# Performance work log

Hardware: AMD Instinct MI355X
Metric: run time of the kernel (lower is better)

## Reference

```python
import jax, jax.numpy as jnp
import numpy as np

B = 64        # graphs per batch
N = 128       # nodes per graph (equal-sized graphs -> static shapes)
EMB = 16      # gm_val feature dim
OUT = 64      # output edge feature dim
E_REAL = 65536
FILL_VALUE = 0.0


def setup_inputs() -> dict:
    key = jax.random.key(0)
    k1, k2, k3, k4, k5 = jax.random.split(key, 5)

    num_nodes = B * N
    batch = jnp.asarray(np.arange(num_nodes) // N, dtype=jnp.int64)

    # gm_index: all within-graph node pairs, row-major per graph (matches full_edge_index order)
    loc = np.arange(N)
    src_l = np.repeat(loc, N)            # [N*N]
    dst_l = np.tile(loc, N)              # [N*N]
    off = (np.arange(B) * N)[:, None]    # [B,1]
    gm_src = (off + src_l[None, :]).reshape(-1)
    gm_dst = (off + dst_l[None, :]).reshape(-1)
    gm_index = jnp.asarray(np.stack([gm_src, gm_dst]), dtype=jnp.int64)  # [2, B*N*N]

    gm_val = jax.random.normal(k1, (B * N * N, EMB), dtype=jnp.float32)

    # real edges: random within each graph, E_REAL/B edges per graph
    eg = E_REAL // B
    src_loc = jax.random.randint(k2, (B, eg), 0, N)
    dst_loc = jax.random.randint(k3, (B, eg), 0, N)
    goff = (jnp.arange(B) * N)[:, None]
    edge_index = jnp.stack([(src_loc + goff).reshape(-1),
                            (dst_loc + goff).reshape(-1)]).astype(jnp.int64)

    edge_attr = jax.random.normal(k4, (E_REAL, OUT), dtype=jnp.float32)

    # fc weight, xavier-uniform-like init, shape [out_dim, emb_dim] (torch Linear layout)
    bound = float(np.sqrt(6.0 / (EMB + OUT)))
    W = jax.random.uniform(k5, (OUT, EMB), minval=-bound, maxval=bound, dtype=jnp.float32)

    return {"batch": batch, "edge_index": edge_index, "edge_attr": edge_attr,
            "gm_index": gm_index, "gm_val": gm_val, "W": W}


def _flat_id(idx):
    # map global (src, dst) within-graph pair to flat position in coalesced
    # (graph-major, row-major) full edge ordering. Graphs are equal-sized.
    src, dst = idx[0], idx[1]
    g = src // N
    return g * (N * N) + (src - g * N) * N + (dst - g * N)


def reference(batch, edge_index, edge_attr, gm_index, gm_val, W):
    total = B * N * N
    # FC(gm_val): [E_gm, EMB] @ [EMB, OUT]
    gm_proj = gm_val @ W.T

    # coalesce(cat([edge_index, gm_index, full_index]), op='add') over equal-sized
    # graphs yields exactly the sorted full pair set; values are scatter-added.
    out_val = jnp.full((total, OUT), FILL_VALUE, dtype=edge_attr.dtype)  # padding for all pairs
    out_val = out_val.at[_flat_id(edge_index)].add(edge_attr)
    out_val = out_val.at[_flat_id(gm_index)].add(gm_proj)

    # coalesced (sorted, deduped) index = full pair set in graph/row-major order
    flat = jnp.arange(total)
    g = flat // (N * N)
    rem = flat % (N * N)
    out_idx = jnp.stack([g * N + rem // N, g * N + rem % N]).astype(edge_index.dtype)
    return out_idx, out_val
```

## Files before the change

### kernel.cpp

```cpp
#include <hip/hip_runtime.h>

#define BGRAPH 64
#define NNODE  128
#define EMB    16
#define OUTF   64
#define EREAL  65536
#define TOTAL  (BGRAPH * NNODE * NNODE)

typedef float floatx4 __attribute__((ext_vector_type(4)));

#define GEMM_BLOCKS 8192
#define ROWS_PER_BLOCK_ITER 32
#define GEMM_ITERS (TOTAL / (GEMM_BLOCKS * ROWS_PER_BLOCK_ITER))

__global__ __launch_bounds__(256) void gemm_rows_kernel(
    const float* __restrict__ gm_val,
    const float* __restrict__ W,
    float* __restrict__ out_val)
{
    const int tid = threadIdx.x;
    const int oq  = tid & 15;
    const int rg  = tid >> 4;

    float w[4][16];
    const floatx4* W4 = (const floatx4*)W + oq * 16;
    #pragma unroll
    for (int j = 0; j < 4; ++j) {
        #pragma unroll
        for (int q = 0; q < 4; ++q) {
            floatx4 t = W4[j * 4 + q];
            w[j][q * 4 + 0] = t.x;
            w[j][q * 4 + 1] = t.y;
            w[j][q * 4 + 2] = t.z;
            w[j][q * 4 + 3] = t.w;
        }
    }

    const int stride = GEMM_BLOCKS * ROWS_PER_BLOCK_ITER;
    int rA = blockIdx.x * ROWS_PER_BLOCK_ITER + rg;
    int rB = rA + 16;

    const floatx4* pA = (const floatx4*)(gm_val + (size_t)rA * EMB);
    const floatx4* pB = (const floatx4*)(gm_val + (size_t)rB * EMB);
    floatx4 c0 = pA[0], c1 = pA[1], c2 = pA[2], c3 = pA[3];
    floatx4 d0 = pB[0], d1 = pB[1], d2 = pB[2], d3 = pB[3];

    #pragma unroll
    for (int it = 0; it < GEMM_ITERS; ++it) {
        floatx4 n0, n1, n2, n3, m0, m1, m2, m3;
        if (it + 1 < GEMM_ITERS) {
            const floatx4* qA = (const floatx4*)(gm_val + (size_t)(rA + stride) * EMB);
            const floatx4* qB = (const floatx4*)(gm_val + (size_t)(rB + stride) * EMB);
            n0 = qA[0]; n1 = qA[1]; n2 = qA[2]; n3 = qA[3];
            m0 = qB[0]; m1 = qB[1]; m2 = qB[2]; m3 = qB[3];
        }

        {
            float v[16] = {c0.x,c0.y,c0.z,c0.w, c1.x,c1.y,c1.z,c1.w,
                           c2.x,c2.y,c2.z,c2.w, c3.x,c3.y,c3.z,c3.w};
            float s0 = 0.f, s1 = 0.f, s2 = 0.f, s3 = 0.f;
            #pragma unroll
            for (int k = 0; k < EMB; ++k) {
                s0 += v[k] * w[0][k];
                s1 += v[k] * w[1][k];
                s2 += v[k] * w[2][k];
                s3 += v[k] * w[3][k];
            }
            floatx4 o = {s0, s1, s2, s3};
            __builtin_nontemporal_store(o, (floatx4*)(out_val + (size_t)rA * OUTF + oq * 4));
        }
        {
            float v[16] = {d0.x,d0.y,d0.z,d0.w, d1.x,d1.y,d1.z,d1.w,
                           d2.x,d2.y,d2.z,d2.w, d3.x,d3.y,d3.z,d3.w};
            float s0 = 0.f, s1 = 0.f, s2 = 0.f, s3 = 0.f;
            #pragma unroll
            for (int k = 0; k < EMB; ++k) {
                s0 += v[k] * w[0][k];
                s1 += v[k] * w[1][k];
                s2 += v[k] * w[2][k];
                s3 += v[k] * w[3][k];
            }
            floatx4 o = {s0, s1, s2, s3};
            __builtin_nontemporal_store(o, (floatx4*)(out_val + (size_t)rB * OUTF + oq * 4));
        }

        c0 = n0; c1 = n1; c2 = n2; c3 = n3;
        d0 = m0; d1 = m1; d2 = m2; d3 = m3;
        rA += stride; rB += stride;
    }
}

#define SCATTER_BLOCKS ((EREAL * OUTF) / 256)
#define IDX_BLOCKS (TOTAL / 256)

__global__ __launch_bounds__(256) void scatter_idx_kernel(
    const int* __restrict__ edge_index,
    const float* __restrict__ edge_attr,
    float* __restrict__ out_val,
    float* __restrict__ out_idx)
{
    int bid = blockIdx.x;
    if (bid < SCATTER_BLOCKS) {
        int idx = bid * 256 + threadIdx.x;
        int e = idx >> 6;
        int o = idx & 63;
        int src = edge_index[e];
        int dst = edge_index[EREAL + e];
        int fid = src * NNODE + (dst & (NNODE - 1));
        float a = __builtin_nontemporal_load(edge_attr + (size_t)e * OUTF + o);
        atomicAdd(out_val + (size_t)fid * OUTF + o, a);
    } else {
        int p = (bid - SCATTER_BLOCKS) * 256 + threadIdx.x;
        int g   = p >> 14;
        int rem = p & 16383;
        out_idx[p]         = (float)(g * NNODE + (rem >> 7));
        out_idx[TOTAL + p] = (float)(g * NNODE + (rem & 127));
    }
}

extern "C" void kernel_launch(void* const* d_in, const int* in_sizes, int n_in,
                              void* d_out, int out_size, void* d_ws, size_t ws_size,
                              hipStream_t stream)
{
    const int*   edge_index = (const int*)d_in[1];
    const float* edge_attr  = (const float*)d_in[2];
    const float* gm_val     = (const float*)d_in[4];
    const float* W          = (const float*)d_in[5];

    float* out      = (float*)d_out;
    float* out_idx  = out;
    float* out_val  = out + (size_t)2 * TOTAL;

    gemm_rows_kernel<<<GEMM_BLOCKS, 256, 0, stream>>>(gm_val, W, out_val);
    scatter_idx_kernel<<<SCATTER_BLOCKS + IDX_BLOCKS, 256, 0, stream>>>(
        edge_index, edge_attr, out_val, out_idx);
}
```

Baseline: 426.7 us.

## Bin real edges per pair and gather them inside the projection kernel

Measured after the change: 467.1 us. 9.5% more time.

```diff
diff --git a/kernel.cpp b/kernel.cpp
--- a/kernel.cpp
+++ b/kernel.cpp
@@ -13,14 +13,69 @@
 #define ROWS_PER_BLOCK_ITER 32
 #define GEMM_ITERS (TOTAL / (GEMM_BLOCKS * ROWS_PER_BLOCK_ITER))
 
-__global__ __launch_bounds__(256) void gemm_rows_kernel(
+#define SLOT_CAP 8
+#define BIN_BLOCKS (EREAL / 256)
+#define IDX_BLOCKS (TOTAL / 256)
+
+__global__ __launch_bounds__(256) void zero_cnt_kernel(uint4* __restrict__ cnt4)
+{
+    cnt4[blockIdx.x * 256 + threadIdx.x] = make_uint4(0u, 0u, 0u, 0u);
+}
+
+__global__ __launch_bounds__(256) void bin_idx_kernel(
+    const int* __restrict__ edge_index,
+    unsigned* __restrict__ cnt,
+    unsigned* __restrict__ slots,
+    float* __restrict__ out_idx)
+{
+    int bid = blockIdx.x;
+    if (bid < BIN_BLOCKS) {
+        int e = bid * 256 + threadIdx.x;
+        int src = edge_index[e];
+        int dst = edge_index[EREAL + e];
+        int fid = src * NNODE + (dst & (NNODE - 1));
+        unsigned pos = atomicAdd(&cnt[fid], 1u);
+        if (pos < SLOT_CAP)
+            slots[(size_t)fid * SLOT_CAP + pos] = (unsigned)e;
+    } else {
+        int p = (bid - BIN_BLOCKS) * 256 + threadIdx.x;
+        int g   = p >> 14;
+        int rem = p & 16383;
+        out_idx[p]         = (float)(g * NNODE + (rem >> 7));
+        out_idx[TOTAL + p] = (float)(g * NNODE + (rem & 127));
+    }
+}
+
+template <bool FUSED>
+__global__ __launch_bounds__(256) void gemm_kernel(
     const float* __restrict__ gm_val,
     const float* __restrict__ W,
+    const unsigned* __restrict__ cnt,
+    const unsigned* __restrict__ slots,
+    const float* __restrict__ edge_attr,
     float* __restrict__ out_val)
 {
     const int tid = threadIdx.x;
     const int oq  = tid & 15;
     const int rg  = tid >> 4;
+
+    const int stride = GEMM_BLOCKS * ROWS_PER_BLOCK_ITER;
+    int rA = blockIdx.x * ROWS_PER_BLOCK_ITER + rg;
+    int rB = rA + 16;
+
+    const floatx4* pA0 = (const floatx4*)(gm_val + (size_t)rA * EMB);
+    const floatx4* pB0 = (const floatx4*)(gm_val + (size_t)rB * EMB);
+    floatx4 c0 = pA0[0], c1 = pA0[1], c2 = pA0[2], c3 = pA0[3];
+    floatx4 d0 = pB0[0], d1 = pB0[1], d2 = pB0[2], d3 = pB0[3];
+    const floatx4* pA1 = (const floatx4*)(gm_val + (size_t)(rA + stride) * EMB);
+    const floatx4* pB1 = (const floatx4*)(gm_val + (size_t)(rB + stride) * EMB);
+    floatx4 n0 = pA1[0], n1 = pA1[1], n2 = pA1[2], n3 = pA1[3];
+    floatx4 m0 = pB1[0], m1 = pB1[1], m2 = pB1[2], m3 = pB1[3];
+    unsigned ca = 0, cb = 0, na = 0, nb = 0;
+    if (FUSED) {
+        ca = cnt[rA];            cb = cnt[rB];
+        na = cnt[rA + stride];   nb = cnt[rB + stride];
+    }
 
     float w[4][16];
     const floatx4* W4 = (const floatx4*)W + oq * 16;
@@ -36,23 +91,16 @@
         }
     }
 
-    const int stride = GEMM_BLOCKS * ROWS_PER_BLOCK_ITER;
-    int rA = blockIdx.x * ROWS_PER_BLOCK_ITER + rg;
-    int rB = rA + 16;
-
-    const floatx4* pA = (const floatx4*)(gm_val + (size_t)rA * EMB);
-    const floatx4* pB = (const floatx4*)(gm_val + (size_t)rB * EMB);
-    floatx4 c0 = pA[0], c1 = pA[1], c2 = pA[2], c3 = pA[3];
-    floatx4 d0 = pB[0], d1 = pB[1], d2 = pB[2], d3 = pB[3];
-
     #pragma unroll
     for (int it = 0; it < GEMM_ITERS; ++it) {
-        floatx4 n0, n1, n2, n3, m0, m1, m2, m3;
-        if (it + 1 < GEMM_ITERS) {
-            const floatx4* qA = (const floatx4*)(gm_val + (size_t)(rA + stride) * EMB);
-            const floatx4* qB = (const floatx4*)(gm_val + (size_t)(rB + stride) * EMB);
-            n0 = qA[0]; n1 = qA[1]; n2 = qA[2]; n3 = qA[3];
-            m0 = qB[0]; m1 = qB[1]; m2 = qB[2]; m3 = qB[3];
+        floatx4 e0, e1, e2, e3, f0, f1, f2, f3;
+        unsigned ea = 0, fb = 0;
+        if (it + 2 < GEMM_ITERS) {
+            const floatx4* qA = (const floatx4*)(gm_val + (size_t)(rA + 2 * stride) * EMB);
+            const floatx4* qB = (const floatx4*)(gm_val + (size_t)(rB + 2 * stride) * EMB);
+            e0 = qA[0]; e1 = qA[1]; e2 = qA[2]; e3 = qA[3];
+            f0 = qB[0]; f1 = qB[1]; f2 = qB[2]; f3 = qB[3];
+            if (FUSED) { ea = cnt[rA + 2 * stride]; fb = cnt[rB + 2 * stride]; }
         }
 
         {
@@ -67,6 +115,13 @@
                 s3 += v[k] * w[3][k];
             }
             floatx4 o = {s0, s1, s2, s3};
+            if (FUSED && ca) {
+                unsigned nE = ca < SLOT_CAP ? ca : SLOT_CAP;
+                for (unsigned i = 0; i < nE; ++i) {
+                    unsigned e = slots[(size_t)rA * SLOT_CAP + i];
+                    o += *(const floatx4*)(edge_attr + (size_t)e * OUTF + oq * 4);
+                }
+            }
             __builtin_nontemporal_store(o, (floatx4*)(out_val + (size_t)rA * OUTF + oq * 4));
         }
         {
@@ -81,17 +136,25 @@
                 s3 += v[k] * w[3][k];
             }
             floatx4 o = {s0, s1, s2, s3};
+            if (FUSED && cb) {
+                unsigned nE = cb < SLOT_CAP ? cb : SLOT_CAP;
+                for (unsigned i = 0; i < nE; ++i) {
+                    unsigned e = slots[(size_t)rB * SLOT_CAP + i];
+                    o += *(const floatx4*)(edge_attr + (size_t)e * OUTF + oq * 4);
+                }
+            }
             __builtin_nontemporal_store(o, (floatx4*)(out_val + (size_t)rB * OUTF + oq * 4));
         }
 
-        c0 = n0; c1 = n1; c2 = n2; c3 = n3;
-        d0 = m0; d1 = m1; d2 = m2; d3 = m3;
+        c0 = n0; c1 = n1; c2 = n2; c3 = n3;  ca = na;
+        d0 = m0; d1 = m1; d2 = m2; d3 = m3;  cb = nb;
+        n0 = e0; n1 = e1; n2 = e2; n3 = e3;  na = ea;
+        m0 = f0; m1 = f1; m2 = f2; m3 = f3;  nb = fb;
         rA += stride; rB += stride;
     }
 }
 
 #define SCATTER_BLOCKS ((EREAL * OUTF) / 256)
-#define IDX_BLOCKS (TOTAL / 256)
 
 __global__ __launch_bounds__(256) void scatter_idx_kernel(
     const int* __restrict__ edge_index,
@@ -131,7 +194,20 @@
     float* out_idx  = out;
     float* out_val  = out + (size_t)2 * TOTAL;
 
-    gemm_rows_kernel<<<GEMM_BLOCKS, 256, 0, stream>>>(gm_val, W, out_val);
-    scatter_idx_kernel<<<SCATTER_BLOCKS + IDX_BLOCKS, 256, 0, stream>>>(
-        edge_index, edge_attr, out_val, out_idx);
-}
+    const size_t ws_need = (size_t)TOTAL * 4 + (size_t)TOTAL * SLOT_CAP * 4;
+
+    if (ws_size >= ws_need) {
+        unsigned* cnt   = (unsigned*)d_ws;
+        unsigned* slots = cnt + TOTAL;
+        zero_cnt_kernel<<<1024, 256, 0, stream>>>((uint4*)cnt);
+        bin_idx_kernel<<<BIN_BLOCKS + IDX_BLOCKS, 256, 0, stream>>>(
+            edge_index, cnt, slots, out_idx);
+        gemm_kernel<true><<<GEMM_BLOCKS, 256, 0, stream>>>(
+            gm_val, W, cnt, slots, edge_attr, out_val);
+    } else {
+        gemm_kernel<false><<<GEMM_BLOCKS, 256, 0, stream>>>(
+            gm_val, W, nullptr, nullptr, nullptr, out_val);
+        scatter_idx_kernel<<<SCATTER_BLOCKS + IDX_BLOCKS, 256, 0, stream>>>(
+            edge_index, edge_attr, out_val, out_idx);
+    }
+}
```

## Bin real edges per pair and fuse their accumulation into the GEMM epilogue

Applied to the files above, without the earlier changes.

Result: faster. 375.9 us (-11.9%).

```diff
diff --git a/kernel.cpp b/kernel.cpp
--- a/kernel.cpp
+++ b/kernel.cpp
@@ -9,18 +9,66 @@
 
 typedef float floatx4 __attribute__((ext_vector_type(4)));
 
-#define GEMM_BLOCKS 8192
-#define ROWS_PER_BLOCK_ITER 32
-#define GEMM_ITERS (TOTAL / (GEMM_BLOCKS * ROWS_PER_BLOCK_ITER))
+#define SLOT_CAP 8
 
-__global__ __launch_bounds__(256) void gemm_rows_kernel(
+__global__ __launch_bounds__(256) void init_kernel(
+    uint4* __restrict__ cnt4,
+    float* __restrict__ out_idx)
+{
+    int t  = blockIdx.x * 256 + threadIdx.x;
+    cnt4[t] = make_uint4(0u, 0u, 0u, 0u);
+
+    int p0  = t * 4;
+    int g   = p0 >> 14;
+    int rem = p0 & 16383;
+    float sv = (float)(g * NNODE + (rem >> 7));
+    float dbase = (float)(g * NNODE + (rem & 127));
+    floatx4 s = {sv, sv, sv, sv};
+    floatx4 d = {dbase, dbase + 1.f, dbase + 2.f, dbase + 3.f};
+    *(floatx4*)(out_idx + p0)          = s;
+    *(floatx4*)(out_idx + TOTAL + p0)  = d;
+}
+
+__global__ __launch_bounds__(256) void bin_kernel(
+    const int* __restrict__ edge_index,
+    unsigned* __restrict__ cnt,
+    unsigned* __restrict__ slots)
+{
+    int e = blockIdx.x * 256 + threadIdx.x;
+    int src = edge_index[e];
+    int dst = edge_index[EREAL + e];
+    int fid = src * NNODE + (dst & (NNODE - 1));
+    unsigned pos = atomicAdd(&cnt[fid], 1u);
+    if (pos < SLOT_CAP)
+        slots[(size_t)fid * SLOT_CAP + pos] = (unsigned)e;
+}
+
+#define CHUNK 256
+#define GEMM_BLOCKS (TOTAL / CHUNK)
+
+template <bool FUSED>
+__global__ __launch_bounds__(256) void gemm_lds_kernel(
     const float* __restrict__ gm_val,
     const float* __restrict__ W,
+    const unsigned* __restrict__ cnt,
+    const unsigned* __restrict__ slots,
+    const float* __restrict__ edge_attr,
     float* __restrict__ out_val)
 {
-    const int tid = threadIdx.x;
-    const int oq  = tid & 15;
-    const int rg  = tid >> 4;
+    __shared__ float lds[CHUNK * EMB];
+    const int tid  = threadIdx.x;
+    const int oq   = tid & 15;
+    const int grp  = tid >> 4;
+    const int base = blockIdx.x * CHUNK;
+
+    const floatx4* src = (const floatx4*)(gm_val + (size_t)base * EMB);
+    floatx4 s0 = src[tid];
+    floatx4 s1 = src[tid + 256];
+    floatx4 s2 = src[tid + 512];
+    floatx4 s3 = src[tid + 768];
+
+    unsigned cv = 0;
+    if (FUSED) cv = cnt[base + grp + 16 * oq];
 
     float w[4][16];
     const floatx4* W4 = (const floatx4*)W + oq * 16;
@@ -36,57 +84,41 @@
         }
     }
 
-    const int stride = GEMM_BLOCKS * ROWS_PER_BLOCK_ITER;
-    int rA = blockIdx.x * ROWS_PER_BLOCK_ITER + rg;
-    int rB = rA + 16;
+    floatx4* ldsf4 = (floatx4*)lds;
+    ldsf4[tid]       = s0;
+    ldsf4[tid + 256] = s1;
+    ldsf4[tid + 512] = s2;
+    ldsf4[tid + 768] = s3;
+    __syncthreads();
 
-    const floatx4* pA = (const floatx4*)(gm_val + (size_t)rA * EMB);
-    const floatx4* pB = (const floatx4*)(gm_val + (size_t)rB * EMB);
-    floatx4 c0 = pA[0], c1 = pA[1], c2 = pA[2], c3 = pA[3];
-    floatx4 d0 = pB[0], d1 = pB[1], d2 = pB[2], d3 = pB[3];
+    for (int s = 0; s < 16; ++s) {
+        const int r = base + grp + 16 * s;
+        const floatx4* rowp = ldsf4 + (size_t)(grp + 16 * s) * 4;
+        floatx4 a = rowp[0], b = rowp[1], c = rowp[2], d = rowp[3];
+        float v[16] = {a.x,a.y,a.z,a.w, b.x,b.y,b.z,b.w,
+                       c.x,c.y,c.z,c.w, d.x,d.y,d.z,d.w};
 
-    #pragma unroll
-    for (int it = 0; it < GEMM_ITERS; ++it) {
-        floatx4 n0, n1, n2, n3, m0, m1, m2, m3;
-        if (it + 1 < GEMM_ITERS) {
-            const floatx4* qA = (const floatx4*)(gm_val + (size_t)(rA + stride) * EMB);
-            const floatx4* qB = (const floatx4*)(gm_val + (size_t)(rB + stride) * EMB);
-            n0 = qA[0]; n1 = qA[1]; n2 = qA[2]; n3 = qA[3];
-            m0 = qB[0]; m1 = qB[1]; m2 = qB[2]; m3 = qB[3];
+        float t0 = 0.f, t1 = 0.f, t2 = 0.f, t3 = 0.f;
+        #pragma unroll
+        for (int k = 0; k < EMB; ++k) {
+            t0 += v[k] * w[0][k];
+            t1 += v[k] * w[1][k];
+            t2 += v[k] * w[2][k];
+            t3 += v[k] * w[3][k];
         }
+        floatx4 o = {t0, t1, t2, t3};
 
-        {
-            float v[16] = {c0.x,c0.y,c0.z,c0.w, c1.x,c1.y,c1.z,c1.w,
-                           c2.x,c2.y,c2.z,c2.w, c3.x,c3.y,c3.z,c3.w};
-            float s0 = 0.f, s1 = 0.f, s2 = 0.f, s3 = 0.f;
-            #pragma unroll
-            for (int k = 0; k < EMB; ++k) {
-                s0 += v[k] * w[0][k];
-                s1 += v[k] * w[1][k];
-                s2 += v[k] * w[2][k];
-                s3 += v[k] * w[3][k];
+        if (FUSED) {
+            unsigned cR = __shfl(cv, s, 16);
+            if (cR) {
+                unsigned nE = cR < SLOT_CAP ? cR : SLOT_CAP;
+                for (unsigned i = 0; i < nE; ++i) {
+                    unsigned e = slots[(size_t)r * SLOT_CAP + i];
+                    o += *(const floatx4*)(edge_attr + (size_t)e * OUTF + oq * 4);
+                }
             }
-            floatx4 o = {s0, s1, s2, s3};
-            __builtin_nontemporal_store(o, (floatx4*)(out_val + (size_t)rA * OUTF + oq * 4));
         }
-        {
-            float v[16] = {d0.x,d0.y,d0.z,d0.w, d1.x,d1.y,d1.z,d1.w,
-                           d2.x,d2.y,d2.z,d2.w, d3.x,d3.y,d3.z,d3.w};
-            float s0 = 0.f, s1 = 0.f, s2 = 0.f, s3 = 0.f;
-            #pragma unroll
-            for (int k = 0; k < EMB; ++k) {
-                s0 += v[k] * w[0][k];
-                s1 += v[k] * w[1][k];
-                s2 += v[k] * w[2][k];
-                s3 += v[k] * w[3][k];
-            }
-            floatx4 o = {s0, s1, s2, s3};
-            __builtin_nontemporal_store(o, (floatx4*)(out_val + (size_t)rB * OUTF + oq * 4));
-        }
-
-        c0 = n0; c1 = n1; c2 = n2; c3 = n3;
-        d0 = m0; d1 = m1; d2 = m2; d3 = m3;
-        rA += stride; rB += stride;
+        __builtin_nontemporal_store(o, (floatx4*)(out_val + (size_t)r * OUTF + oq * 4));
     }
 }
 
@@ -131,7 +163,19 @@
     float* out_idx  = out;
     float* out_val  = out + (size_t)2 * TOTAL;
 
-    gemm_rows_kernel<<<GEMM_BLOCKS, 256, 0, stream>>>(gm_val, W, out_val);
-    scatter_idx_kernel<<<SCATTER_BLOCKS + IDX_BLOCKS, 256, 0, stream>>>(
-        edge_index, edge_attr, out_val, out_idx);
+    const size_t ws_need = (size_t)TOTAL * 4 + (size_t)TOTAL * SLOT_CAP * 4;
+
+    if (ws_size >= ws_need) {
+        unsigned* cnt   = (unsigned*)d_ws;
+        unsigned* slots = cnt + TOTAL;
+        init_kernel<<<TOTAL / 4 / 256, 256, 0, stream>>>((uint4*)cnt, out_idx);
+        bin_kernel<<<EREAL / 256, 256, 0, stream>>>(edge_index, cnt, slots);
+        gemm_lds_kernel<true><<<GEMM_BLOCKS, 256, 0, stream>>>(
+            gm_val, W, cnt, slots, edge_attr, out_val);
+    } else {
+        gemm_lds_kernel<false><<<GEMM_BLOCKS, 256, 0, stream>>>(
+            gm_val, W, nullptr, nullptr, nullptr, out_val);
+        scatter_idx_kernel<<<SCATTER_BLOCKS + IDX_BLOCKS, 256, 0, stream>>>(
+            edge_index, edge_attr, out_val, out_idx);
+    }
 }
```
